# Kernel tuning notes

Hardware: AMD Instinct MI355X
Metric: run time of the kernel (lower is better)

Reference implementation:

```python
import jax, jax.numpy as jnp
import numpy as np

B, N, D, L = 8, 2048, 1024, 128


def setup_inputs() -> dict:
    key = jax.random.key(0)
    ks = jax.random.split(key, 8)
    return {
        "e_i_t_minus_1": jax.random.normal(ks[0], (B, D), dtype=jnp.float32),
        "e_j_t": jax.random.normal(ks[1], (B, N, D), dtype=jnp.float32),
        "imp_j_t": jax.random.uniform(ks[2], (B, N), dtype=jnp.float32),
        "R_lk": jax.random.normal(ks[3], (L, D), dtype=jnp.float32),
        "W_q": jax.random.normal(ks[4], (D, D), dtype=jnp.float32) * (D ** -0.5),
        "W_k": jax.random.normal(ks[5], (D, D), dtype=jnp.float32) * (D ** -0.5),
        "W_v": jax.random.normal(ks[6], (D, D), dtype=jnp.float32) * (D ** -0.5),
        "omega": jax.random.normal(ks[7], (D,), dtype=jnp.float32),
    }


def reference(e_i_t_minus_1, e_j_t, imp_j_t, R_lk, W_q, W_k, W_v, omega):
    # torch nn.Linear(x) = x @ W.T  (weights stored [out, in])
    q_i = jnp.einsum('bd,ed->be', e_i_t_minus_1, W_q)[:, None, :]   # [B,1,D]
    k_j = jnp.einsum('bnd,ed->bne', e_j_t, W_k)                      # [B,N,D]
    sigma = jnp.einsum('bnd,d->bn', jnp.tanh(q_i + k_j), omega)      # [B,N]
    exp_sigma = jnp.exp(sigma)
    sum_exp = jnp.sum(exp_sigma, axis=1, keepdims=True)              # [B,1]
    a_ij = imp_j_t * exp_sigma / (sum_exp + 1e-9)                    # [B,N]
    v_j = jnp.einsum('bnd,ed->bne', e_j_t, W_v)                      # [B,N,D]
    A = jnp.einsum('bn,bnd->bd', a_ij, v_j)                          # [B,D]
    # R_lk[l,d] * a_ij[b,n] * v_j[b,n,d], summed over n -> [B,L,D]
    A_lk = jnp.einsum('bn,bnd,ld->bld', a_ij, v_j, R_lk)             # [B,L,D]
    A_l = A                                                          # identical math in source
    return (A, A_lk, A_l)
```

## Files before the change

kernel.cpp:

```cpp
#include <hip/hip_runtime.h>
#include <hip/hip_bf16.h>
#include <math.h>

#define BB 8
#define NN 2048
#define DD 1024
#define LL 128
#define MM (BB*NN)

typedef _Float16 half8 __attribute__((ext_vector_type(8)));
typedef _Float16 half4 __attribute__((ext_vector_type(4)));
typedef __attribute__((ext_vector_type(4))) float floatx4;

__device__ __forceinline__ void glds16(const void* g, void* l) {
    __builtin_amdgcn_global_load_lds(
        (const __attribute__((address_space(1))) unsigned int*)g,
        (__attribute__((address_space(3))) unsigned int*)l, 16, 0, 0);
}

#define CFENCE() asm volatile("" ::: "memory")
#define BARRIER() do { CFENCE(); __builtin_amdgcn_s_barrier(); CFENCE(); } while (0)

__device__ __forceinline__ float ftanh(float x) {
    float e = __expf(2.0f * x);
    return 1.0f - 2.0f * __builtin_amdgcn_rcpf(e + 1.0f);
}

__global__ __launch_bounds__(256) void prep_kernel(const float* __restrict__ e_j,
                                                   _Float16* __restrict__ eh,
                                                   const float* __restrict__ Wk,
                                                   _Float16* __restrict__ wh,
                                                   const float* __restrict__ e_i,
                                                   const float* __restrict__ Wq,
                                                   float* __restrict__ q) {
    __shared__ float us[BB][DD];
    int blk = blockIdx.x;
    int tid = threadIdx.x;
    if (blk < 8192) {
        int i = blk * 256 + tid;
        const float4* xp = (const float4*)e_j + (size_t)i * 2;
        float4 v0 = xp[0], v1 = xp[1];
        half8 h;
        h[0] = (_Float16)v0.x; h[1] = (_Float16)v0.y;
        h[2] = (_Float16)v0.z; h[3] = (_Float16)v0.w;
        h[4] = (_Float16)v1.x; h[5] = (_Float16)v1.y;
        h[6] = (_Float16)v1.z; h[7] = (_Float16)v1.w;
        *(half8*)(eh + (size_t)i * 8) = h;
    } else if (blk < 8704) {
        int i = (blk - 8192) * 256 + tid;
        const float4* xp = (const float4*)Wk + (size_t)i * 2;
        float4 v0 = xp[0], v1 = xp[1];
        half8 h;
        h[0] = (_Float16)v0.x; h[1] = (_Float16)v0.y;
        h[2] = (_Float16)v0.z; h[3] = (_Float16)v0.w;
        h[4] = (_Float16)v1.x; h[5] = (_Float16)v1.y;
        h[6] = (_Float16)v1.z; h[7] = (_Float16)v1.w;
        *(half8*)(wh + (size_t)i * 8) = h;
    } else {
        for (int i = tid; i < BB * DD / 4; i += 256)
            ((float4*)&us[0][0])[i] = ((const float4*)e_i)[i];
        __syncthreads();
        int w = tid >> 6, lane = tid & 63;
        int d = (blk - 8704) * 4 + w;
        float acc[8] = {0.f, 0.f, 0.f, 0.f, 0.f, 0.f, 0.f, 0.f};
        for (int e0 = 0; e0 < DD; e0 += 256) {
            float4 wv = *(const float4*)&Wq[(size_t)d * DD + e0 + lane * 4];
            #pragma unroll
            for (int r = 0; r < 8; ++r) {
                float4 uv = *(const float4*)&us[r][e0 + lane * 4];
                acc[r] += wv.x * uv.x + wv.y * uv.y + wv.z * uv.z + wv.w * uv.w;
            }
        }
        #pragma unroll
        for (int r = 0; r < 8; ++r) {
            float s = acc[r];
            #pragma unroll
            for (int off = 32; off; off >>= 1) s += __shfl_down(s, off, 64);
            if (lane == 0) q[r * DD + d] = s;
        }
    }
}

__global__ __launch_bounds__(512, 2) void sigma256(const _Float16* __restrict__ eh,
                                                   const _Float16* __restrict__ wh,
                                                   const float* __restrict__ q,
                                                   const float* __restrict__ omega,
                                                   float* __restrict__ sig_part)
{
    __shared__ _Float16 As[4][256][32];
    __shared__ _Float16 Bs[4][256][32];

    const int tid  = threadIdx.x;
    const int lane = tid & 63;
    const int wid  = tid >> 6;
    const int wr   = wid >> 2;
    const int wc   = wid & 3;
    const int c15  = lane & 15, quad = lane >> 4;

    const int wgid   = (blockIdx.x & 7) * 32 + (blockIdx.x >> 3);
    const int colBlk = wgid >> 6;
    const int rowBlk = wgid & 63;
    const int row0   = rowBlk * 256;
    const int col0   = colBlk * 256;
    const int b      = row0 / NN;

    const int srow = wid * 16 + (lane >> 2);
    const int ssub = ((lane & 3) ^ ((lane >> 3) & 3)) * 8;
    const _Float16* gA = eh + (size_t)(row0 + srow) * DD + ssub;
    const _Float16* gB = wh + (size_t)(col0 + srow) * DD + ssub;
    char* const ldsA0 = (char*)&As[0][0][0] + wid * 1024;
    char* const ldsB0 = (char*)&Bs[0][0][0] + wid * 1024;

#define STAGE_A(kt) do { int _bi = (kt) & 3; int _k0 = (kt) * 32;                  \
        glds16(gA + _k0,                    ldsA0 + _bi * 16384);                  \
        glds16(gA + (size_t)128 * DD + _k0, ldsA0 + _bi * 16384 + 8192); } while (0)
#define STAGE_B(kt) do { int _bi = (kt) & 3; int _k0 = (kt) * 32;                  \
        glds16(gB + _k0,                    ldsB0 + _bi * 16384);                  \
        glds16(gB + (size_t)128 * DD + _k0, ldsB0 + _bi * 16384 + 8192); } while (0)

    const char* const Abase = (const char*)&As[0][0][0];
    const char* const Bbase = (const char*)&Bs[0][0][0];
#define FRAG(base, bi, row, qd) \
    (*(const half8*)((base) + (bi) * 16384 + (row) * 64 + ((((qd) ^ (((row) >> 1) & 3))) << 4)))

    floatx4 acc[8][4];
    #pragma unroll
    for (int m = 0; m < 8; ++m)
        #pragma unroll
        for (int n = 0; n < 4; ++n) acc[m][n] = (floatx4){0.f, 0.f, 0.f, 0.f};

    STAGE_A(0); STAGE_B(0);
    STAGE_A(1); STAGE_B(1);
    STAGE_A(2); STAGE_B(2);
    asm volatile("s_waitcnt vmcnt(8)" ::: "memory");
    BARRIER();

#define TILE_BODY(t_, DO_STAGE, VMW)                                              \
    {                                                                             \
        const int bi = (t_) & 3;                                                  \
        half8 a[4], bb[4];                                                        \
        _Pragma("unroll")                                                         \
        for (int m = 0; m < 4; ++m) a[m]  = FRAG(Abase, bi, wr * 128 + m * 16 + c15, quad); \
        _Pragma("unroll")                                                         \
        for (int n = 0; n < 4; ++n) bb[n] = FRAG(Bbase, bi, wc * 64  + n * 16 + c15, quad); \
        if (DO_STAGE) STAGE_A((t_) + 3);                                          \
        BARRIER();                                                                \
        __builtin_amdgcn_s_setprio(1);                                            \
        _Pragma("unroll")                                                         \
        for (int m = 0; m < 4; ++m)                                               \
            _Pragma("unroll")                                                     \
            for (int n = 0; n < 4; ++n)                                           \
                acc[m][n] = __builtin_amdgcn_mfma_f32_16x16x32_f16(a[m], bb[n], acc[m][n], 0, 0, 0); \
        __builtin_amdgcn_s_setprio(0);                                            \
        BARRIER();                                                                \
        _Pragma("unroll")                                                         \
        for (int m = 0; m < 4; ++m) a[m] = FRAG(Abase, bi, wr * 128 + 64 + m * 16 + c15, quad); \
        if (DO_STAGE) STAGE_B((t_) + 3);                                          \
        BARRIER();                                                                \
        __builtin_amdgcn_s_setprio(1);                                            \
        _Pragma("unroll")                                                         \
        for (int m = 0; m < 4; ++m)                                               \
            _Pragma("unroll")                                                     \
            for (int n = 0; n < 4; ++n)                                           \
                acc[4 + m][n] = __builtin_amdgcn_mfma_f32_16x16x32_f16(a[m], bb[n], acc[4 + m][n], 0, 0, 0); \
        __builtin_amdgcn_s_setprio(0);                                            \
        asm volatile("s_waitcnt vmcnt(" #VMW ")" ::: "memory");                   \
        BARRIER();                                                                \
    }

    for (int t = 0; t < 29; ++t) TILE_BODY(t, 1, 8)
    TILE_BODY(29, 0, 4)
    TILE_BODY(30, 0, 0)
    TILE_BODY(31, 0, 0)

    float part[8][4];
    #pragma unroll
    for (int m = 0; m < 8; ++m)
        #pragma unroll
        for (int r = 0; r < 4; ++r) part[m][r] = 0.f;

    #pragma unroll
    for (int n = 0; n < 4; ++n) {
        int col = col0 + wc * 64 + n * 16 + c15;
        float qv = q[b * DD + col];
        float om = omega[col];
        #pragma unroll
        for (int m = 0; m < 8; ++m)
            #pragma unroll
            for (int r = 0; r < 4; ++r)
                part[m][r] += ftanh(acc[m][n][r] + qv) * om;
    }

    float (*red)[4] = (float(*)[4])&As[0][0][0];
    #pragma unroll
    for (int m = 0; m < 8; ++m)
        #pragma unroll
        for (int r = 0; r < 4; ++r) {
            float s = part[m][r];
            s += __shfl_xor(s, 1, 64);
            s += __shfl_xor(s, 2, 64);
            s += __shfl_xor(s, 4, 64);
            s += __shfl_xor(s, 8, 64);
            if (c15 == 0) red[wr * 128 + m * 16 + quad * 4 + r][wc] = s;
        }
    __syncthreads();
    if (tid < 256)
        sig_part[(size_t)colBlk * MM + row0 + tid] =
            red[tid][0] + red[tid][1] + red[tid][2] + red[tid][3];
#undef TILE_BODY
#undef FRAG
#undef STAGE_A
#undef STAGE_B
}

__global__ __launch_bounds__(256) void softmax_k(const float* __restrict__ sig_part,
                                                 const float* __restrict__ imp,
                                                 float* __restrict__ a_ij) {
    int b = blockIdx.x >> 3, slice = blockIdx.x & 7;
    int tid = threadIdx.x;
    __shared__ float red[256];
    float sv[8];
    float m = -1e30f;
    #pragma unroll
    for (int p = 0; p < 8; ++p) {
        int n = p * 256 + tid;
        float s = 0.f;
        #pragma unroll
        for (int db = 0; db < 4; ++db) s += sig_part[db * MM + b * NN + n];
        sv[p] = s;
        m = fmaxf(m, s);
    }
    red[tid] = m; __syncthreads();
    for (int off = 128; off; off >>= 1) {
        if (tid < off) red[tid] = fmaxf(red[tid], red[tid + off]);
        __syncthreads();
    }
    m = red[0]; __syncthreads();
    float sum = 0.f;
    #pragma unroll
    for (int p = 0; p < 8; ++p) sum += expf(sv[p] - m);
    red[tid] = sum; __syncthreads();
    for (int off = 128; off; off >>= 1) {
        if (tid < off) red[tid] += red[tid + off];
        __syncthreads();
    }
    float inv = 1.f / (red[0] + 1e-9f * expf(-m));
    int n = slice * 256 + tid;
    a_ij[b * NN + n] = imp[b * NN + n] * expf(sv[slice] - m) * inv;
}

__global__ __launch_bounds__(256) void u_kernel(const float* __restrict__ a_ij,
                                                const _Float16* __restrict__ eh,
                                                float* __restrict__ u_part) {
    int b = blockIdx.x >> 7, nc = blockIdx.x & 127;
    int t = threadIdx.x;
    float4 acc = {0.f, 0.f, 0.f, 0.f};
    const _Float16* base = eh + ((size_t)(b * NN + nc * 16)) * DD + t * 4;
    const float* ap = a_ij + b * NN + nc * 16;
    #pragma unroll
    for (int n = 0; n < 16; ++n) {
        float a = ap[n];
        half4 v = *(const half4*)(base + (size_t)n * DD);
        acc.x += a * (float)v[0]; acc.y += a * (float)v[1];
        acc.z += a * (float)v[2]; acc.w += a * (float)v[3];
    }
    *(float4*)(u_part + ((size_t)nc * BB + b) * DD + t * 4) = acc;
}

__global__ __launch_bounds__(256) void ureduce(const float* __restrict__ u_part,
                                               float* __restrict__ u) {
    int i = blockIdx.x * 256 + threadIdx.x;
    float s = 0.f;
    #pragma unroll 8
    for (int nc = 0; nc < 128; ++nc) s += u_part[(size_t)nc * BB * DD + i];
    u[i] = s;
}

__global__ __launch_bounds__(256) void rowdot8(const float* __restrict__ X,
                                               const float* __restrict__ W,
                                               float* __restrict__ out) {
    __shared__ float us[BB][DD];
    int tid = threadIdx.x;
    for (int i = tid; i < BB * DD / 4; i += 256)
        ((float4*)&us[0][0])[i] = ((const float4*)X)[i];
    __syncthreads();
    int w = tid >> 6, lane = tid & 63;
    int d = blockIdx.x * 4 + w;
    float acc[8] = {0.f, 0.f, 0.f, 0.f, 0.f, 0.f, 0.f, 0.f};
    for (int e0 = 0; e0 < DD; e0 += 256) {
        float4 wv = *(const float4*)&W[(size_t)d * DD + e0 + lane * 4];
        #pragma unroll
        for (int r = 0; r < 8; ++r) {
            float4 uv = *(const float4*)&us[r][e0 + lane * 4];
            acc[r] += wv.x * uv.x + wv.y * uv.y + wv.z * uv.z + wv.w * uv.w;
        }
    }
    #pragma unroll
    for (int r = 0; r < 8; ++r) {
        float s = acc[r];
        #pragma unroll
        for (int off = 32; off; off >>= 1) s += __shfl_down(s, off, 64);
        if (lane == 0) out[r * DD + d] = s;
    }
}

__global__ __launch_bounds__(256) void out_kernel(const float* __restrict__ A,
                                                  const float* __restrict__ Rlk,
                                                  float* __restrict__ out) {
    int i = blockIdx.x * 256 + threadIdx.x;
    int d = i & (DD - 1);
    int l = (i >> 10) & (LL - 1);
    int b = i >> 17;
    out[BB * DD + i] = A[b * DD + d] * Rlk[l * DD + d];
    if (i < BB * DD) {
        out[i] = A[i];
        out[BB * DD + BB * LL * DD + i] = A[i];
    }
}

extern "C" void kernel_launch(void* const* d_in, const int* in_sizes, int n_in,
                              void* d_out, int out_size, void* d_ws, size_t ws_size,
                              hipStream_t stream) {
    const float* e_i   = (const float*)d_in[0];
    const float* e_j   = (const float*)d_in[1];
    const float* imp   = (const float*)d_in[2];
    const float* Rlk   = (const float*)d_in[3];
    const float* Wq    = (const float*)d_in[4];
    const float* Wk    = (const float*)d_in[5];
    const float* Wv    = (const float*)d_in[6];
    const float* omega = (const float*)d_in[7];
    float* out = (float*)d_out;
    float* ws  = (float*)d_ws;

    float* q    = ws;
    float* sigp = ws + 8192;
    float* a_ij = ws + 139264;
    float* u    = ws + 155648;
    _Float16* eh = (_Float16*)(ws + 172032);
    _Float16* wh = eh + (size_t)MM * DD;
    float* u_part = (float*)(wh + (size_t)DD * DD);

    prep_kernel<<<8960, 256, 0, stream>>>(e_j, eh, Wk, wh, e_i, Wq, q);

    sigma256<<<dim3(256), 512, 0, stream>>>(eh, wh, q, omega, sigp);

    softmax_k<<<64, 256, 0, stream>>>(sigp, imp, a_ij);

    u_kernel<<<1024, 256, 0, stream>>>(a_ij, eh, u_part);
    ureduce<<<32, 256, 0, stream>>>(u_part, u);

    rowdot8<<<256, 256, 0, stream>>>(u, Wv, a_ij);

    out_kernel<<<(BB * LL * DD) / 256, 256, 0, stream>>>(a_ij, Rlk, out);
}
```

Before: 189.8 us.

## Restructure GEMM main loop to prefetch next-tile fragments and halve barriers

The k-loop of the fused attention-score GEMM is rewritten into two phases per tile, with one barrier per tile instead of four. LDS fragment reads for the next tile (B and the first A half) are issued before the current tile's second MFMA batch, and the second A half is read during the first batch. This software-pipelines LDS reads against MFMA work and cuts barrier stalls. In exchange it raises register pressure from the extra fragment buffers, and the reduced barrier count is a correctness risk for the 4-slot LDS ring.

```diff
diff --git a/kernel.cpp b/kernel.cpp
--- a/kernel.cpp
+++ b/kernel.cpp
@@ -17,9 +17,6 @@
         (const __attribute__((address_space(1))) unsigned int*)g,
         (__attribute__((address_space(3))) unsigned int*)l, 16, 0, 0);
 }
-
-#define CFENCE() asm volatile("" ::: "memory")
-#define BARRIER() do { CFENCE(); __builtin_amdgcn_s_barrier(); CFENCE(); } while (0)
 
 __device__ __forceinline__ float ftanh(float x) {
     float e = __expf(2.0f * x);
@@ -129,49 +126,82 @@
         #pragma unroll
         for (int n = 0; n < 4; ++n) acc[m][n] = (floatx4){0.f, 0.f, 0.f, 0.f};
 
+    half8 a03[4], a47[4], bb[4], bbn[4];
+
     STAGE_A(0); STAGE_B(0);
     STAGE_A(1); STAGE_B(1);
     STAGE_A(2); STAGE_B(2);
     asm volatile("s_waitcnt vmcnt(8)" ::: "memory");
-    BARRIER();
-
-#define TILE_BODY(t_, DO_STAGE, VMW)                                              \
-    {                                                                             \
-        const int bi = (t_) & 3;                                                  \
-        half8 a[4], bb[4];                                                        \
-        _Pragma("unroll")                                                         \
-        for (int m = 0; m < 4; ++m) a[m]  = FRAG(Abase, bi, wr * 128 + m * 16 + c15, quad); \
-        _Pragma("unroll")                                                         \
-        for (int n = 0; n < 4; ++n) bb[n] = FRAG(Bbase, bi, wc * 64  + n * 16 + c15, quad); \
-        if (DO_STAGE) STAGE_A((t_) + 3);                                          \
-        BARRIER();                                                                \
-        __builtin_amdgcn_s_setprio(1);                                            \
-        _Pragma("unroll")                                                         \
-        for (int m = 0; m < 4; ++m)                                               \
-            _Pragma("unroll")                                                     \
-            for (int n = 0; n < 4; ++n)                                           \
-                acc[m][n] = __builtin_amdgcn_mfma_f32_16x16x32_f16(a[m], bb[n], acc[m][n], 0, 0, 0); \
-        __builtin_amdgcn_s_setprio(0);                                            \
-        BARRIER();                                                                \
-        _Pragma("unroll")                                                         \
-        for (int m = 0; m < 4; ++m) a[m] = FRAG(Abase, bi, wr * 128 + 64 + m * 16 + c15, quad); \
-        if (DO_STAGE) STAGE_B((t_) + 3);                                          \
-        BARRIER();                                                                \
-        __builtin_amdgcn_s_setprio(1);                                            \
-        _Pragma("unroll")                                                         \
-        for (int m = 0; m < 4; ++m)                                               \
-            _Pragma("unroll")                                                     \
-            for (int n = 0; n < 4; ++n)                                           \
-                acc[4 + m][n] = __builtin_amdgcn_mfma_f32_16x16x32_f16(a[m], bb[n], acc[4 + m][n], 0, 0, 0); \
-        __builtin_amdgcn_s_setprio(0);                                            \
-        asm volatile("s_waitcnt vmcnt(" #VMW ")" ::: "memory");                   \
-        BARRIER();                                                                \
-    }
-
-    for (int t = 0; t < 29; ++t) TILE_BODY(t, 1, 8)
-    TILE_BODY(29, 0, 4)
-    TILE_BODY(30, 0, 0)
-    TILE_BODY(31, 0, 0)
+    __builtin_amdgcn_s_barrier();
+    __builtin_amdgcn_sched_barrier(0);
+    #pragma unroll
+    for (int n = 0; n < 4; ++n) bb[n]  = FRAG(Bbase, 0, wc * 64  + n * 16 + c15, quad);
+    #pragma unroll
+    for (int m = 0; m < 4; ++m) a03[m] = FRAG(Abase, 0, wr * 128 + m * 16 + c15, quad);
+
+#define PH1(t_, DO_STAGE)                                                          \
+    {                                                                              \
+        const int bi = (t_) & 3;                                                   \
+        _Pragma("unroll")                                                          \
+        for (int m = 0; m < 4; ++m)                                                \
+            a47[m] = FRAG(Abase, bi, wr * 128 + 64 + m * 16 + c15, quad);          \
+        if (DO_STAGE) STAGE_A((t_) + 3);                                           \
+        __builtin_amdgcn_sched_barrier(0);                                         \
+        __builtin_amdgcn_s_setprio(1);                                             \
+        _Pragma("unroll")                                                          \
+        for (int m = 0; m < 4; ++m)                                                \
+            _Pragma("unroll")                                                      \
+            for (int n = 0; n < 4; ++n)                                            \
+                acc[m][n] = __builtin_amdgcn_mfma_f32_16x16x32_f16(a03[m], bb[n], acc[m][n], 0, 0, 0); \
+        __builtin_amdgcn_s_setprio(0);                                             \
+    }
+
+#define PH2(t_, DO_STAGE, DO_READS, VMW)                                           \
+    {                                                                              \
+        const int bin = ((t_) + 1) & 3;                                            \
+        asm volatile("s_waitcnt vmcnt(" #VMW ")" ::: "memory");                    \
+        asm volatile("s_waitcnt lgkmcnt(0)" ::: "memory");                         \
+        __builtin_amdgcn_s_barrier();                                              \
+        __builtin_amdgcn_sched_barrier(0);                                         \
+        if (DO_READS) {                                                            \
+            _Pragma("unroll")                                                      \
+            for (int n = 0; n < 4; ++n)                                            \
+                bbn[n] = FRAG(Bbase, bin, wc * 64  + n * 16 + c15, quad);          \
+            _Pragma("unroll")                                                      \
+            for (int m = 0; m < 4; ++m)                                            \
+                a03[m] = FRAG(Abase, bin, wr * 128 + m * 16 + c15, quad);          \
+        }                                                                          \
+        if (DO_STAGE) STAGE_B((t_) + 3);                                           \
+        __builtin_amdgcn_sched_barrier(0);                                         \
+        __builtin_amdgcn_s_setprio(1);                                             \
+        _Pragma("unroll")                                                          \
+        for (int m = 0; m < 4; ++m)                                                \
+            _Pragma("unroll")                                                      \
+            for (int n = 0; n < 4; ++n)                                            \
+                acc[4 + m][n] = __builtin_amdgcn_mfma_f32_16x16x32_f16(a47[m], bb[n], acc[4 + m][n], 0, 0, 0); \
+        __builtin_amdgcn_s_setprio(0);                                             \
+        if (DO_READS) {                                                            \
+            _Pragma("unroll")                                                      \
+            for (int n = 0; n < 4; ++n) bb[n] = bbn[n];                            \
+        }                                                                          \
+    }
+
+    for (int tt = 0; tt < 28; tt += 4) {
+        PH1(tt + 0, 1) PH2(tt + 0, 1, 1, 6)
+        PH1(tt + 1, 1) PH2(tt + 1, 1, 1, 6)
+        PH1(tt + 2, 1) PH2(tt + 2, 1, 1, 6)
+        PH1(tt + 3, 1) PH2(tt + 3, 1, 1, 6)
+    }
+    PH1(28, 1) PH2(28, 1, 1, 6)
+    PH1(29, 0) PH2(29, 0, 1, 4)
+    PH1(30, 0) PH2(30, 0, 1, 0)
+    PH1(31, 0) PH2(31, 0, 0, 0)
+
+#undef PH1
+#undef PH2
+#undef FRAG
+#undef STAGE_A
+#undef STAGE_B
 
     float part[8][4];
     #pragma unroll
@@ -207,10 +237,6 @@
     if (tid < 256)
         sig_part[(size_t)colBlk * MM + row0 + tid] =
             red[tid][0] + red[tid][1] + red[tid][2] + red[tid][3];
-#undef TILE_BODY
-#undef FRAG
-#undef STAGE_A
-#undef STAGE_B
 }
 
 __global__ __launch_bounds__(256) void softmax_k(const float* __restrict__ sig_part,
```

Result: no change. 191.4 us (+0.8%).

## Restructure sigma GEMM mainloop into 2-stage BK=64 ping-pong with four phases

Applied to the files above, without the earlier changes.

The sigma GEMM's K-loop changes from a 4-deep pipeline of 32-wide K tiles to a 2-stage double buffer of 64-wide K tiles split into 128-row halves. Each K tile now runs as four phases that interleave LDS fragment loads, async global-to-LDS staging and 16-MFMA bursts, separated by sched_barrier and explicit lgkmcnt waits. The LDS swizzle becomes an 8-way XOR to suit the 128-byte rows. The goal is fewer barriers per unit of MFMA work and better overlap of loads with compute, at the cost of a shallower prefetch depth and more hand-scheduled sync that is easy to get wrong.

```diff
diff --git a/kernel.cpp b/kernel.cpp
--- a/kernel.cpp
+++ b/kernel.cpp
@@ -17,9 +17,6 @@
         (const __attribute__((address_space(1))) unsigned int*)g,
         (__attribute__((address_space(3))) unsigned int*)l, 16, 0, 0);
 }
-
-#define CFENCE() asm volatile("" ::: "memory")
-#define BARRIER() do { CFENCE(); __builtin_amdgcn_s_barrier(); CFENCE(); } while (0)
 
 __device__ __forceinline__ float ftanh(float x) {
     float e = __expf(2.0f * x);
@@ -87,14 +84,14 @@
                                                    const float* __restrict__ omega,
                                                    float* __restrict__ sig_part)
 {
-    __shared__ _Float16 As[4][256][32];
-    __shared__ _Float16 Bs[4][256][32];
+    __shared__ _Float16 As[2][2][128][64];
+    __shared__ _Float16 Bs[2][2][128][64];
 
     const int tid  = threadIdx.x;
     const int lane = tid & 63;
     const int wid  = tid >> 6;
-    const int wr   = wid >> 2;
-    const int wc   = wid & 3;
+    const int wm   = wid >> 2;
+    const int wn   = wid & 3;
     const int c15  = lane & 15, quad = lane >> 4;
 
     const int wgid   = (blockIdx.x & 7) * 32 + (blockIdx.x >> 3);
@@ -104,24 +101,28 @@
     const int col0   = colBlk * 256;
     const int b      = row0 / NN;
 
-    const int srow = wid * 16 + (lane >> 2);
-    const int ssub = ((lane & 3) ^ ((lane >> 3) & 3)) * 8;
-    const _Float16* gA = eh + (size_t)(row0 + srow) * DD + ssub;
-    const _Float16* gB = wh + (size_t)(col0 + srow) * DD + ssub;
-    char* const ldsA0 = (char*)&As[0][0][0] + wid * 1024;
-    char* const ldsB0 = (char*)&Bs[0][0][0] + wid * 1024;
-
-#define STAGE_A(kt) do { int _bi = (kt) & 3; int _k0 = (kt) * 32;                  \
-        glds16(gA + _k0,                    ldsA0 + _bi * 16384);                  \
-        glds16(gA + (size_t)128 * DD + _k0, ldsA0 + _bi * 16384 + 8192); } while (0)
-#define STAGE_B(kt) do { int _bi = (kt) & 3; int _k0 = (kt) * 32;                  \
-        glds16(gB + _k0,                    ldsB0 + _bi * 16384);                  \
-        glds16(gB + (size_t)128 * DD + _k0, ldsB0 + _bi * 16384 + 8192); } while (0)
-
-    const char* const Abase = (const char*)&As[0][0][0];
-    const char* const Bbase = (const char*)&Bs[0][0][0];
-#define FRAG(base, bi, row, qd) \
-    (*(const half8*)((base) + (bi) * 16384 + (row) * 64 + ((((qd) ^ (((row) >> 1) & 3))) << 4)))
+    const int l3  = lane >> 3;
+    const int qst = ((lane & 7) ^ l3) * 8;
+    const _Float16* gA = eh + (size_t)(row0 + wid * 16 + l3) * DD + qst;
+    const _Float16* gB = wh + (size_t)(col0 + wid * 16 + l3) * DD + qst;
+    char* const ldsA = (char*)&As[0][0][0][0] + wid * 2048;
+    char* const ldsB = (char*)&Bs[0][0][0][0] + wid * 2048;
+
+#define STG_A(kt, hf, s) do { \
+    glds16(gA + (size_t)(hf) * 128 * DD + (kt) * 64,          ldsA + (s) * 32768 + (hf) * 16384); \
+    glds16(gA + (size_t)(hf) * 128 * DD + (kt) * 64 + 8 * DD, ldsA + (s) * 32768 + (hf) * 16384 + 1024); } while (0)
+#define STG_B(kt, hf, s) do { \
+    glds16(gB + (size_t)(hf) * 128 * DD + (kt) * 64,          ldsB + (s) * 32768 + (hf) * 16384); \
+    glds16(gB + (size_t)(hf) * 128 * DD + (kt) * 64 + 8 * DD, ldsB + (s) * 32768 + (hf) * 16384 + 1024); } while (0)
+
+    const int swz = c15 & 7;
+    const int q0  = (quad ^ swz) << 4;
+    const int q1  = ((4 + quad) ^ swz) << 4;
+    const char* const afp = (const char*)&As[0][0][0][0] + wm * 16384 + c15 * 128;
+    const char* const bfp = (const char*)&Bs[0][0][0][0] + (wn >> 1) * 16384
+                            + ((wn & 1) * 64 + c15) * 128;
+#define FA(s, m, ks) (*(const half8*)(afp + (s) * 32768 + (m) * 2048 + ((ks) ? q1 : q0)))
+#define FB(s, n, ks) (*(const half8*)(bfp + (s) * 32768 + (n) * 2048 + ((ks) ? q1 : q0)))
 
     floatx4 acc[8][4];
     #pragma unroll
@@ -129,49 +130,68 @@
         #pragma unroll
         for (int n = 0; n < 4; ++n) acc[m][n] = (floatx4){0.f, 0.f, 0.f, 0.f};
 
-    STAGE_A(0); STAGE_B(0);
-    STAGE_A(1); STAGE_B(1);
-    STAGE_A(2); STAGE_B(2);
-    asm volatile("s_waitcnt vmcnt(8)" ::: "memory");
-    BARRIER();
-
-#define TILE_BODY(t_, DO_STAGE, VMW)                                              \
-    {                                                                             \
-        const int bi = (t_) & 3;                                                  \
-        half8 a[4], bb[4];                                                        \
-        _Pragma("unroll")                                                         \
-        for (int m = 0; m < 4; ++m) a[m]  = FRAG(Abase, bi, wr * 128 + m * 16 + c15, quad); \
-        _Pragma("unroll")                                                         \
-        for (int n = 0; n < 4; ++n) bb[n] = FRAG(Bbase, bi, wc * 64  + n * 16 + c15, quad); \
-        if (DO_STAGE) STAGE_A((t_) + 3);                                          \
-        BARRIER();                                                                \
-        __builtin_amdgcn_s_setprio(1);                                            \
-        _Pragma("unroll")                                                         \
-        for (int m = 0; m < 4; ++m)                                               \
-            _Pragma("unroll")                                                     \
-            for (int n = 0; n < 4; ++n)                                           \
-                acc[m][n] = __builtin_amdgcn_mfma_f32_16x16x32_f16(a[m], bb[n], acc[m][n], 0, 0, 0); \
-        __builtin_amdgcn_s_setprio(0);                                            \
-        BARRIER();                                                                \
-        _Pragma("unroll")                                                         \
-        for (int m = 0; m < 4; ++m) a[m] = FRAG(Abase, bi, wr * 128 + 64 + m * 16 + c15, quad); \
-        if (DO_STAGE) STAGE_B((t_) + 3);                                          \
-        BARRIER();                                                                \
-        __builtin_amdgcn_s_setprio(1);                                            \
-        _Pragma("unroll")                                                         \
-        for (int m = 0; m < 4; ++m)                                               \
-            _Pragma("unroll")                                                     \
-            for (int n = 0; n < 4; ++n)                                           \
-                acc[4 + m][n] = __builtin_amdgcn_mfma_f32_16x16x32_f16(a[m], bb[n], acc[4 + m][n], 0, 0, 0); \
-        __builtin_amdgcn_s_setprio(0);                                            \
-        asm volatile("s_waitcnt vmcnt(" #VMW ")" ::: "memory");                   \
-        BARRIER();                                                                \
-    }
-
-    for (int t = 0; t < 29; ++t) TILE_BODY(t, 1, 8)
-    TILE_BODY(29, 0, 4)
-    TILE_BODY(30, 0, 0)
-    TILE_BODY(31, 0, 0)
+    half8 a[8], bl[4], bh[4];
+
+#define BARx()  __builtin_amdgcn_s_barrier()
+#define SBARx() __builtin_amdgcn_sched_barrier(0)
+#define LGKM0() asm volatile("s_waitcnt lgkmcnt(0)" ::: "memory")
+#define MFMA16(MB, NB, BARR) \
+    __builtin_amdgcn_s_setprio(1); \
+    _Pragma("unroll") for (int m_ = 0; m_ < 4; ++m_) \
+    _Pragma("unroll") for (int n_ = 0; n_ < 2; ++n_) \
+    _Pragma("unroll") for (int ks_ = 0; ks_ < 2; ++ks_) \
+        acc[(MB) + m_][(NB) + n_] = __builtin_amdgcn_mfma_f32_16x16x32_f16( \
+            a[m_ * 2 + ks_], BARR[n_ * 2 + ks_], acc[(MB) + m_][(NB) + n_], 0, 0, 0); \
+    __builtin_amdgcn_s_setprio(0);
+
+#define PH_A(s, STAGE) \
+    _Pragma("unroll") for (int m_ = 0; m_ < 4; ++m_) { a[m_*2] = FA(s, m_, 0); a[m_*2+1] = FA(s, m_, 1); } \
+    _Pragma("unroll") for (int n_ = 0; n_ < 2; ++n_) { bl[n_*2] = FB(s, n_, 0); bl[n_*2+1] = FB(s, n_, 1); } \
+    STAGE; SBARx(); BARx(); LGKM0(); SBARx(); MFMA16(0, 0, bl) BARx();
+#define PH_B(s, STAGE) \
+    _Pragma("unroll") for (int n_ = 0; n_ < 2; ++n_) { bh[n_*2] = FB(s, 2+n_, 0); bh[n_*2+1] = FB(s, 2+n_, 1); } \
+    STAGE; SBARx(); BARx(); LGKM0(); SBARx(); MFMA16(0, 2, bh) BARx();
+#define PH_C(s, STAGE) \
+    _Pragma("unroll") for (int m_ = 0; m_ < 4; ++m_) { a[m_*2] = FA(s, 4+m_, 0); a[m_*2+1] = FA(s, 4+m_, 1); } \
+    STAGE; SBARx(); BARx(); LGKM0(); SBARx(); MFMA16(4, 0, bl) BARx();
+#define PH_D(s, STAGE, VMW) \
+    STAGE; SBARx(); BARx(); LGKM0(); SBARx(); MFMA16(4, 2, bh) \
+    asm volatile("s_waitcnt vmcnt(" VMW ")" ::: "memory"); BARx();
+
+    STG_A(0, 0, 0); STG_A(0, 1, 0); STG_B(0, 0, 0); STG_B(0, 1, 0);
+    STG_B(1, 0, 1); STG_B(1, 1, 1);
+    asm volatile("s_waitcnt vmcnt(4)" ::: "memory");
+    BARx();
+
+    for (int i = 0; i < 7; ++i) {
+        const int k1 = 2 * i + 1, k2 = 2 * i + 2, k3 = 2 * i + 3;
+        PH_A(0, STG_A(k1, 0, 1))
+        PH_B(0, STG_A(k1, 1, 1))
+        PH_C(0, STG_B(k2, 0, 0))
+        PH_D(0, STG_B(k2, 1, 0), "4")
+        PH_A(1, STG_A(k2, 0, 0))
+        PH_B(1, STG_A(k2, 1, 0))
+        PH_C(1, STG_B(k3, 0, 1))
+        PH_D(1, STG_B(k3, 1, 1), "4")
+    }
+    PH_A(0, STG_A(15, 0, 1))
+    PH_B(0, STG_A(15, 1, 1))
+    PH_C(0, ((void)0))
+    PH_D(0, ((void)0), "0")
+    PH_A(1, ((void)0))
+    PH_B(1, ((void)0))
+    PH_C(1, ((void)0))
+    PH_D(1, ((void)0), "0")
+
+#undef PH_A
+#undef PH_B
+#undef PH_C
+#undef PH_D
+#undef MFMA16
+#undef FA
+#undef FB
+#undef STG_A
+#undef STG_B
 
     float part[8][4];
     #pragma unroll
@@ -181,7 +201,7 @@
 
     #pragma unroll
     for (int n = 0; n < 4; ++n) {
-        int col = col0 + wc * 64 + n * 16 + c15;
+        int col = col0 + wn * 64 + n * 16 + c15;
         float qv = q[b * DD + col];
         float om = omega[col];
         #pragma unroll
@@ -191,7 +211,7 @@
                 part[m][r] += ftanh(acc[m][n][r] + qv) * om;
     }
 
-    float (*red)[4] = (float(*)[4])&As[0][0][0];
+    float (*red)[4] = (float(*)[4])&As[0][0][0][0];
     #pragma unroll
     for (int m = 0; m < 8; ++m)
         #pragma unroll
@@ -201,16 +221,12 @@
             s += __shfl_xor(s, 2, 64);
             s += __shfl_xor(s, 4, 64);
             s += __shfl_xor(s, 8, 64);
-            if (c15 == 0) red[wr * 128 + m * 16 + quad * 4 + r][wc] = s;
+            if (c15 == 0) red[wm * 128 + m * 16 + quad * 4 + r][wn] = s;
         }
     __syncthreads();
     if (tid < 256)
         sig_part[(size_t)colBlk * MM + row0 + tid] =
             red[tid][0] + red[tid][1] + red[tid][2] + red[tid][3];
-#undef TILE_BODY
-#undef FRAG
-#undef STAGE_A
-#undef STAGE_B
 }
 
 __global__ __launch_bounds__(256) void softmax_k(const float* __restrict__ sig_part,
```

Result: faster. 185.0 us (-2.5%).
